# Optimization experiments

Hardware: AMD Instinct MI355X
Metric: run time of the kernel (lower is better)

## Reference

```python
import jax, jax.numpy as jnp
import numpy as np

H = 4          # num attention heads
C1 = 64        # channel_num[0]
C2 = 128       # channel_num[1]
KV = C1 + C2   # 192
MLP = C1 * 4   # expand_ratio=4


def _layernorm(x, g, b, eps=1e-6):
    m = jnp.mean(x, axis=-1, keepdims=True)
    v = jnp.mean((x - m) ** 2, axis=-1, keepdims=True)
    return (x - m) * jax.lax.rsqrt(v + eps) * g + b


def setup_inputs() -> dict:
    key = jax.random.key(0)
    ks = jax.random.split(key, 12)
    B, N = 8, 3136
    s_q = 1.0 / np.sqrt(C1)
    s_kv = 1.0 / np.sqrt(KV)
    return {
        "emb1": jax.random.normal(ks[0], (B, N, C1), jnp.float32),
        "emb2": jax.random.normal(ks[1], (B, N, C2), jnp.float32),
        # per-head projection weights (nn.Linear convention: y = x @ W.T)
        "Wq": jax.random.uniform(ks[2], (H, C1, C1), jnp.float32, -s_q, s_q),
        "Wk": jax.random.uniform(ks[3], (H, KV, KV), jnp.float32, -s_kv, s_kv),
        "Wv": jax.random.uniform(ks[4], (H, KV, KV), jnp.float32, -s_kv, s_kv),
        "Wout": jax.random.uniform(ks[5], (C1, C1), jnp.float32, -s_q, s_q),
        "ln1_g": jnp.ones((C1,), jnp.float32),
        "ln1_b": jnp.zeros((C1,), jnp.float32),
        "lnall_g": jnp.ones((KV,), jnp.float32),
        "lnall_b": jnp.zeros((KV,), jnp.float32),
        "ffn_g": jnp.ones((C1,), jnp.float32),
        "ffn_b": jnp.zeros((C1,), jnp.float32),
        "fc1_w": jax.random.uniform(ks[6], (MLP, C1), jnp.float32, -s_q, s_q),
        "fc1_b": jnp.zeros((MLP,), jnp.float32),
        "fc2_w": jax.random.uniform(ks[7], (C1, MLP), jnp.float32, -1.0 / np.sqrt(MLP), 1.0 / np.sqrt(MLP)),
        "fc2_b": jnp.zeros((C1,), jnp.float32),
    }


def reference(emb1, emb2, Wq, Wk, Wv, Wout, ln1_g, ln1_b, lnall_g, lnall_b,
              ffn_g, ffn_b, fc1_w, fc1_b, fc2_w, fc2_b):
    # emb1: [B,N,C1], emb2: [B,N,C2]
    emb_all = jnp.concatenate([emb1, emb2], axis=2)          # [B,N,KV]
    cx1 = _layernorm(emb1, ln1_g, ln1_b)                     # [B,N,C1]
    ea = _layernorm(emb_all, lnall_g, lnall_b)               # [B,N,KV]

    # batched per-head projections (replaces Python loop over ModuleList)
    qT = jnp.einsum('bnc,hdc->bhdn', cx1, Wq)                # [B,H,C1,N]
    k = jnp.einsum('bnk,hdk->bhnd', ea, Wk)                  # [B,H,N,KV]
    vT = jnp.einsum('bnk,hdk->bhdn', ea, Wv)                 # [B,H,KV,N]

    scores = jnp.einsum('bhcn,bhnk->bhck', qT, k) / np.sqrt(KV)  # [B,H,C1,KV]
    # InstanceNorm2d over spatial dims (C1, KV) per (batch, head), affine=False
    m = jnp.mean(scores, axis=(2, 3), keepdims=True)
    v = jnp.mean((scores - m) ** 2, axis=(2, 3), keepdims=True)
    scores = (scores - m) * jax.lax.rsqrt(v + 1e-5)
    probs = jax.nn.softmax(scores, axis=3)                   # softmax over KV

    ctx = jnp.einsum('bhck,bhkn->bhcn', probs, vT)           # [B,H,C1,N]
    ctx = jnp.mean(ctx, axis=1).transpose(0, 2, 1)           # mean over heads -> [B,N,C1]
    o = ctx @ Wout.T                                         # [B,N,C1]

    cx = emb1 + o                                            # residual
    x = _layernorm(cx, ffn_g, ffn_b)
    x = jax.nn.gelu(x @ fc1_w.T + fc1_b, approximate=False)
    x = x @ fc2_w.T + fc2_b
    return x + cx
```

## Files before the change

kernel.cpp:

```cpp
#include <hip/hip_runtime.h>
#include <hip/hip_bf16.h>

typedef __hip_bfloat16 bf;
typedef unsigned short ushort_t;
typedef __attribute__((ext_vector_type(8))) short short8;
typedef __attribute__((ext_vector_type(4))) float f32x4;

#define NB 8
#define SEQ 3136
#define HD 4
#define ZS 6

__device__ __forceinline__ float lo_bf(unsigned u){ return __uint_as_float(u << 16); }
__device__ __forceinline__ float hi_bf(unsigned u){ return __uint_as_float(u & 0xffff0000u); }
__device__ __forceinline__ float b16f(ushort_t s){ return __uint_as_float(((unsigned)s) << 16); }
__device__ __forceinline__ unsigned short f2bfbits(float f){
  unsigned u = __float_as_uint(f);
  unsigned r = u + 0x7fffu + ((u >> 16) & 1u);
  return (unsigned short)(r >> 16);
}
__device__ __forceinline__ float ldin(const void* p, long i, bool isbf){
  return isbf ? __bfloat162float(((const bf*)p)[i]) : ((const float*)p)[i];
}
__device__ __forceinline__ ushort_t cvt1(const void* p, long i, bool isbf){
  return isbf ? ((const ushort_t*)p)[i] : f2bfbits(((const float*)p)[i]);
}
#define DTYPE_FLAG(p) (((const unsigned*)(p))[0] == 0x3F803F80u)

__device__ __forceinline__ float wsum(float v){
  #pragma unroll
  for (int o = 32; o > 0; o >>= 1) v += __shfl_xor(v, o, 64);
  return v;
}

__global__ __launch_bounds__(256) void k_g(
    const void* __restrict__ emb1, const void* __restrict__ emb2,
    const void* __restrict__ g1, const void* __restrict__ b1,
    const void* __restrict__ ga, const void* __restrict__ ba,
    const void* __restrict__ Wq, const void* __restrict__ Wk, const void* __restrict__ Wv,
    const void* __restrict__ f1w, const void* __restrict__ f2w, const void* __restrict__ Wout,
    ushort_t* __restrict__ part, ushort_t* __restrict__ eag,
    ushort_t* __restrict__ Wqb, ushort_t* __restrict__ Wkb, ushort_t* __restrict__ WvTb,
    ushort_t* __restrict__ f1wb, ushort_t* __restrict__ f2wb,
    ushort_t* __restrict__ Woutb, unsigned* __restrict__ cnt){
  bool isbf = DTYPE_FLAG(g1);
  int tid = threadIdx.x;
  int b = blockIdx.y, ch = blockIdx.x;
  if (ch >= 49){
    if (b != 0) return;
    int g = (ch - 49)*256 + tid;
    const int STR = 24*256;
    if (g < 8) cnt[g] = 0;
    for (int i = g; i < 16384; i += STR) Wqb[i] = cvt1(Wq, i, isbf);
    for (int i = g; i < 4096;  i += STR) Woutb[i] = cvt1(Wout, i, isbf);
    for (int i = g; i < 147456; i += STR) Wkb[i] = cvt1(Wk, i, isbf);
    for (int i = g; i < 147456; i += STR){
      int hh = i / 36864, r = i - hh*36864;
      int j = r / 192, e = r - j*192;
      WvTb[i] = cvt1(Wv, (long)hh*36864 + e*192 + j, isbf);
    }
    for (int i = g; i < 16384; i += STR) f1wb[i] = cvt1(f1w, i, isbf);
    for (int i = g; i < 16384; i += STR) f2wb[i] = cvt1(f2w, i, isbf);
    return;
  }
  __shared__ __align__(16) ushort_t z1t[64*72];
  __shared__ __align__(16) ushort_t zat[192*72];
  int wave = tid >> 6, lane = tid & 63;
  int quad = lane >> 4, nl = lane & 15;
  long t0 = (long)b*SEQ + ch*64;
  float g1l = ldin(g1,lane,isbf), b1l = ldin(b1,lane,isbf);
  float ga0 = ldin(ga,lane,isbf),     ba0 = ldin(ba,lane,isbf);
  float ga1 = ldin(ga,64+lane,isbf),  ba1 = ldin(ba,64+lane,isbf);
  float ga2 = ldin(ga,128+lane,isbf), ba2 = ldin(ba,128+lane,isbf);
  #pragma unroll 4
  for (int k = 0; k < 16; ++k){
    int tok = wave*16 + k;
    long t = t0 + tok;
    float e1  = ldin(emb1, t*64 + lane, isbf);
    float e2a = ldin(emb2, t*128 + lane, isbf);
    float e2b = ldin(emb2, t*128 + 64 + lane, isbf);
    float s1 = wsum(e1), ss1 = wsum(e1*e1);
    float m1 = s1*(1.f/64.f);
    float r1 = rsqrtf(fmaxf(ss1*(1.f/64.f) - m1*m1, 0.f) + 1e-6f);
    z1t[lane*72 + tok] = f2bfbits((e1 - m1)*r1*g1l + b1l);
    float s23 = wsum(e2a+e2b), ss23 = wsum(e2a*e2a + e2b*e2b);
    float ma = (s1+s23)*(1.f/192.f);
    float ra = rsqrtf(fmaxf((ss1+ss23)*(1.f/192.f) - ma*ma, 0.f) + 1e-6f);
    unsigned short za0 = f2bfbits((e1  - ma)*ra*ga0 + ba0);
    unsigned short za1 = f2bfbits((e2a - ma)*ra*ga1 + ba1);
    unsigned short za2 = f2bfbits((e2b - ma)*ra*ga2 + ba2);
    zat[lane*72 + tok]       = za0;
    zat[(64+lane)*72 + tok]  = za1;
    zat[(128+lane)*72 + tok] = za2;
    eag[t*192 + lane]       = za0;
    eag[t*192 + 64 + lane]  = za1;
    eag[t*192 + 128 + lane] = za2;
  }
  __syncthreads();
  short8 a0 = *reinterpret_cast<const short8*>(&z1t[(wave*16+nl)*72 + quad*8]);
  short8 a1 = *reinterpret_cast<const short8*>(&z1t[(wave*16+nl)*72 + 32 + quad*8]);
  ushort_t* P = part + ((long)b*49 + ch)*12288;
  #pragma unroll
  for (int nt = 0; nt < 12; ++nt){
    f32x4 cd = {0.f,0.f,0.f,0.f};
    short8 b0 = *reinterpret_cast<const short8*>(&zat[(nt*16+nl)*72 + quad*8]);
    cd = __builtin_amdgcn_mfma_f32_16x16x32_bf16(a0, b0, cd, 0, 0, 0);
    short8 b1v = *reinterpret_cast<const short8*>(&zat[(nt*16+nl)*72 + 32 + quad*8]);
    cd = __builtin_amdgcn_mfma_f32_16x16x32_bf16(a1, b1v, cd, 0, 0, 0);
    #pragma unroll
    for (int reg = 0; reg < 4; ++reg)
      P[(wave*16 + quad*4 + reg)*192 + nt*16 + nl] = f2bfbits(cd[reg]);
  }
}

__global__ __launch_bounds__(64) void k_red(
    const ushort_t* __restrict__ part, ushort_t* __restrict__ Gb){
  int idx4 = blockIdx.x*64 + threadIdx.x;
  int b = idx4 / 3072, e4 = idx4 - b*3072;
  const ushort_t* p = part + (long)b*49*12288 + e4*4;
  float s0=0.f, s1=0.f, s2=0.f, s3=0.f;
  #pragma unroll
  for (int ch = 0; ch < 49; ++ch){
    uint2 u = *reinterpret_cast<const uint2*>(p + (long)ch*12288);
    s0 += lo_bf(u.x); s1 += hi_bf(u.x); s2 += lo_bf(u.y); s3 += hi_bf(u.y);
  }
  unsigned lo = (unsigned)f2bfbits(s0) | ((unsigned)f2bfbits(s1) << 16);
  unsigned hi = (unsigned)f2bfbits(s2) | ((unsigned)f2bfbits(s3) << 16);
  *reinterpret_cast<uint2*>(Gb + (long)idx4*4) = make_uint2(lo, hi);
}

__global__ __launch_bounds__(256) void k_att(
    const ushort_t* __restrict__ Gb, const ushort_t* __restrict__ Wqb,
    const ushort_t* __restrict__ Wkb, const ushort_t* __restrict__ WvTb,
    const ushort_t* __restrict__ Woutb,
    float* __restrict__ Mh, unsigned* __restrict__ cnt, ushort_t* __restrict__ W2){
  __shared__ __align__(16) ushort_t sT[192*72];
  __shared__ __align__(16) ushort_t sPh[64*200];
  __shared__ __align__(16) ushort_t sPl[64*200];
  __shared__ float red[8];
  __shared__ float stat[2];
  __shared__ unsigned sOld;
  int h = blockIdx.x, b = blockIdx.y, z = blockIdx.z;
  int tid = threadIdx.x, wave = tid >> 6, lane = tid & 63;
  int quad = lane >> 4, nl = lane & 15;

  const ushort_t* Gp = Gb + (long)b*12288;
  short8 aG[6];
  #pragma unroll
  for (int ks = 0; ks < 6; ++ks)
    aG[ks] = *reinterpret_cast<const short8*>(Gp + (wave*16+nl)*192 + ks*32 + quad*8);
  const ushort_t* Wkp = Wkb + (long)h*36864;
  short8 bcur[6], bnxt[6];
  #pragma unroll
  for (int ks = 0; ks < 6; ++ks)
    bcur[ks] = *reinterpret_cast<const short8*>(Wkp + (long)nl*192 + ks*32 + quad*8);
  #pragma unroll
  for (int nt = 0; nt < 12; ++nt){
    if (nt < 11){
      #pragma unroll
      for (int ks = 0; ks < 6; ++ks)
        bnxt[ks] = *reinterpret_cast<const short8*>(Wkp + (long)((nt+1)*16+nl)*192 + ks*32 + quad*8);
    }
    f32x4 cd = {0.f,0.f,0.f,0.f};
    #pragma unroll
    for (int ks = 0; ks < 6; ++ks)
      cd = __builtin_amdgcn_mfma_f32_16x16x32_bf16(aG[ks], bcur[ks], cd, 0, 0, 0);
    #pragma unroll
    for (int reg = 0; reg < 4; ++reg)
      sT[(nt*16+nl)*72 + wave*16 + quad*4 + reg] = f2bfbits(cd[reg]);
    #pragma unroll
    for (int ks = 0; ks < 6; ++ks) bcur[ks] = bnxt[ks];
  }
  __syncthreads();

  const ushort_t* Wqp = Wqb + (long)h*4096;
  short8 aQ[2];
  #pragma unroll
  for (int ks = 0; ks < 2; ++ks)
    aQ[ks] = *reinterpret_cast<const short8*>(Wqp + (wave*16+nl)*64 + ks*32 + quad*8);
  const float scale = 0.07216878364870323f;
  float sv[12][4];
  float ps = 0.f, pss = 0.f;
  #pragma unroll
  for (int nt = 0; nt < 12; ++nt){
    f32x4 cd = {0.f,0.f,0.f,0.f};
    #pragma unroll
    for (int ks = 0; ks < 2; ++ks){
      short8 bt = *reinterpret_cast<const short8*>(&sT[(nt*16+nl)*72 + ks*32 + quad*8]);
      cd = __builtin_amdgcn_mfma_f32_16x16x32_bf16(aQ[ks], bt, cd, 0, 0, 0);
    }
    #pragma unroll
    for (int reg = 0; reg < 4; ++reg){
      float v = cd[reg]*scale;
      sv[nt][reg] = v;
      ps += v; pss += v*v;
    }
  }
  ps = wsum(ps); pss = wsum(pss);
  if (lane == 0){ red[wave] = ps; red[4+wave] = pss; }
  __syncthreads();
  if (tid == 0){
    float s  = red[0]+red[1]+red[2]+red[3];
    float s2 = red[4]+red[5]+red[6]+red[7];
    float m = s * (1.f/12288.f);
    stat[0] = m;
    stat[1] = rsqrtf(fmaxf(s2*(1.f/12288.f) - m*m, 0.f) + 1e-5f);
  }
  __syncthreads();

  const ushort_t* Wvp = WvTb + (long)h*36864;
  short8 bv[2][6];
  #pragma unroll
  for (int ntl = 0; ntl < 2; ++ntl)
    #pragma unroll
    for (int ks = 0; ks < 6; ++ks)
      bv[ntl][ks] = *reinterpret_cast<const short8*>(Wvp + (long)((z*2+ntl)*16+nl)*192 + ks*32 + quad*8);

  float m = stat[0], r = stat[1];
  #pragma unroll
  for (int reg = 0; reg < 4; ++reg){
    float mx = -3.4e38f;
    #pragma unroll
    for (int nt = 0; nt < 12; ++nt){
      float v = (sv[nt][reg] - m)*r;
      sv[nt][reg] = v;
      mx = fmaxf(mx, v);
    }
    #pragma unroll
    for (int o = 1; o < 16; o <<= 1) mx = fmaxf(mx, __shfl_xor(mx, o, 64));
    float sum = 0.f;
    #pragma unroll
    for (int nt = 0; nt < 12; ++nt){
      float e = __expf(sv[nt][reg] - mx);
      sv[nt][reg] = e;
      sum += e;
    }
    #pragma unroll
    for (int o = 1; o < 16; o <<= 1) sum += __shfl_xor(sum, o, 64);
    float inv = 1.f / sum;
    int row = wave*16 + quad*4 + reg;
    #pragma unroll
    for (int nt = 0; nt < 12; ++nt){
      float e = sv[nt][reg]*inv;
      ushort_t hi = f2bfbits(e);
      sPh[row*200 + nt*16 + nl] = hi;
      sPl[row*200 + nt*16 + nl] = f2bfbits(e - b16f(hi));
    }
  }
  __syncthreads();

  short8 aPh[6], aPl[6];
  #pragma unroll
  for (int ks = 0; ks < 6; ++ks){
    aPh[ks] = *reinterpret_cast<const short8*>(&sPh[(wave*16+nl)*200 + ks*32 + quad*8]);
    aPl[ks] = *reinterpret_cast<const short8*>(&sPl[(wave*16+nl)*200 + ks*32 + quad*8]);
  }
  float* Mb = Mh + ((long)b*HD + h)*12288;
  #pragma unroll
  for (int ntl = 0; ntl < 2; ++ntl){
    int nt = z*2 + ntl;
    f32x4 cdh = {0.f,0.f,0.f,0.f};
    f32x4 cdl = {0.f,0.f,0.f,0.f};
    #pragma unroll
    for (int ks = 0; ks < 6; ++ks){
      cdl = __builtin_amdgcn_mfma_f32_16x16x32_bf16(aPl[ks], bv[ntl][ks], cdl, 0, 0, 0);
      cdh = __builtin_amdgcn_mfma_f32_16x16x32_bf16(aPh[ks], bv[ntl][ks], cdh, 0, 0, 0);
    }
    #pragma unroll
    for (int reg = 0; reg < 4; ++reg)
      Mb[(wave*16 + quad*4 + reg)*192 + nt*16 + nl] = cdh[reg] + cdl[reg];
  }

  __threadfence();
  if (tid == 0) sOld = atomicAdd(&cnt[b], 1u);
  __syncthreads();
  if (sOld == HD*ZS - 1u){
    __threadfence();
    const float* M0 = Mh + (long)b*HD*12288;
    for (int g = tid; g < 3072; g += 256){
      float4 x0 = ((const float4*)M0)[g];
      float4 x1 = ((const float4*)(M0 + 12288))[g];
      float4 x2 = ((const float4*)(M0 + 24576))[g];
      float4 x3 = ((const float4*)(M0 + 36864))[g];
      int e = g*4; int c = e/192, j = e - c*192;
      sT[(j+0)*72 + c] = f2bfbits(0.25f*(x0.x+x1.x+x2.x+x3.x));
      sT[(j+1)*72 + c] = f2bfbits(0.25f*(x0.y+x1.y+x2.y+x3.y));
      sT[(j+2)*72 + c] = f2bfbits(0.25f*(x0.z+x1.z+x2.z+x3.z));
      sT[(j+3)*72 + c] = f2bfbits(0.25f*(x0.w+x1.w+x2.w+x3.w));
    }
    __syncthreads();
    short8 aW[2];
    #pragma unroll
    for (int ks = 0; ks < 2; ++ks)
      aW[ks] = *reinterpret_cast<const short8*>(Woutb + (wave*16+nl)*64 + ks*32 + quad*8);
    ushort_t* W2b = W2 + (long)b*12288;
    #pragma unroll
    for (int nt = 0; nt < 12; ++nt){
      f32x4 cd = {0.f,0.f,0.f,0.f};
      #pragma unroll
      for (int ks = 0; ks < 2; ++ks){
        short8 bm = *reinterpret_cast<const short8*>(&sT[(nt*16+nl)*72 + ks*32 + quad*8]);
        cd = __builtin_amdgcn_mfma_f32_16x16x32_bf16(aW[ks], bm, cd, 0, 0, 0);
      }
      #pragma unroll
      for (int reg = 0; reg < 4; ++reg)
        W2b[(wave*16 + quad*4 + reg)*192 + nt*16 + nl] = f2bfbits(cd[reg]);
    }
  }
}

__global__ __launch_bounds__(256) void k_tail(
    const void* __restrict__ emb1, const ushort_t* __restrict__ eag,
    const ushort_t* __restrict__ W2g,
    const void* __restrict__ ffg, const void* __restrict__ ffb,
    const ushort_t* __restrict__ f1wb, const void* __restrict__ f1b,
    const ushort_t* __restrict__ f2wb, const void* __restrict__ f2b,
    const void* __restrict__ lng, void* __restrict__ out){
  bool isbf = DTYPE_FLAG(lng);
  __shared__ __align__(16) ushort_t sCX[16*72];
  __shared__ __align__(16) ushort_t sX[16*88];
  __shared__ __align__(16) ushort_t sH[16*280];
  int tid = threadIdx.x, wave = tid >> 6, lane = tid & 63;
  int quad = lane >> 4, nl = lane & 15;
  int b = blockIdx.y;
  long tbase = (long)b*SEQ + blockIdx.x*16;

  short8 aO[6];
  #pragma unroll
  for (int kt = 0; kt < 6; ++kt)
    aO[kt] = *reinterpret_cast<const short8*>(eag + (tbase + nl)*192 + kt*32 + quad*8);
  const ushort_t* W2b = W2g + (long)b*12288;
  {
    f32x4 cd = {0.f,0.f,0.f,0.f};
    #pragma unroll
    for (int kt = 0; kt < 6; ++kt){
      short8 bf8 = *reinterpret_cast<const short8*>(W2b + (wave*16+nl)*192 + kt*32 + quad*8);
      cd = __builtin_amdgcn_mfma_f32_16x16x32_bf16(aO[kt], bf8, cd, 0, 0, 0);
    }
    #pragma unroll
    for (int reg = 0; reg < 4; ++reg){
      int tokl = quad*4 + reg;
      int chn = wave*16 + nl;
      float e1v = ldin(emb1, (tbase + tokl)*64 + chn, isbf);
      sCX[tokl*72 + chn] = f2bfbits(cd[reg] + e1v);
    }
  }
  __syncthreads();

  float gl = ldin(ffg, lane, isbf), bl = ldin(ffb, lane, isbf);
  #pragma unroll
  for (int k = 0; k < 4; ++k){
    int tokl = wave*4 + k;
    float c = b16f(sCX[tokl*72 + lane]);
    float s = wsum(c), ss = wsum(c*c);
    float m = s*(1.f/64.f);
    float r = rsqrtf(fmaxf(ss*(1.f/64.f) - m*m, 0.f) + 1e-6f);
    sX[tokl*88 + lane] = f2bfbits((c - m)*r*gl + bl);
  }
  __syncthreads();

  short8 aX[2];
  #pragma unroll
  for (int kt = 0; kt < 2; ++kt)
    aX[kt] = *reinterpret_cast<const short8*>(&sX[nl*88 + kt*32 + quad*8]);
  #pragma unroll
  for (int nn = 0; nn < 4; ++nn){
    int nt = wave*4 + nn;
    f32x4 cd = {0.f,0.f,0.f,0.f};
    #pragma unroll
    for (int kt = 0; kt < 2; ++kt){
      short8 bf8 = *reinterpret_cast<const short8*>(f1wb + (long)(nt*16+nl)*64 + kt*32 + quad*8);
      cd = __builtin_amdgcn_mfma_f32_16x16x32_bf16(aX[kt], bf8, cd, 0, 0, 0);
    }
    float bb = ldin(f1b, nt*16+nl, isbf);
    #pragma unroll
    for (int reg = 0; reg < 4; ++reg){
      float v = cd[reg] + bb;
      float h = 0.5f*v*(1.f + erff(v*0.70710678118654752f));
      sH[(quad*4 + reg)*280 + nt*16 + nl] = f2bfbits(h);
    }
  }
  __syncthreads();

  short8 aH[8];
  #pragma unroll
  for (int kt = 0; kt < 8; ++kt)
    aH[kt] = *reinterpret_cast<const short8*>(&sH[nl*280 + kt*32 + quad*8]);
  {
    f32x4 cd = {0.f,0.f,0.f,0.f};
    #pragma unroll
    for (int kt = 0; kt < 8; ++kt){
      short8 bf8 = *reinterpret_cast<const short8*>(f2wb + (long)(wave*16+nl)*256 + kt*32 + quad*8);
      cd = __builtin_amdgcn_mfma_f32_16x16x32_bf16(aH[kt], bf8, cd, 0, 0, 0);
    }
    float bb2 = ldin(f2b, wave*16+nl, isbf);
    #pragma unroll
    for (int reg = 0; reg < 4; ++reg){
      int tokl = quad*4 + reg;
      int chn = wave*16 + nl;
      float y = cd[reg] + bb2 + b16f(sCX[tokl*72 + chn]);
      if (isbf) sCX[tokl*72 + chn] = f2bfbits(y);
      else ((float*)out)[(tbase + tokl)*64 + chn] = y;
    }
  }
  if (isbf){
    __syncthreads();
    int tokl = wave*4 + (lane >> 4), prt = lane & 15;
    uint2 v = *reinterpret_cast<const uint2*>(&sCX[tokl*72 + prt*4]);
    *reinterpret_cast<uint2*>((ushort_t*)out + (tbase + tokl)*64 + prt*4) = v;
  }
}

extern "C" void kernel_launch(void* const* d_in, const int* in_sizes, int n_in,
                              void* d_out, int out_size, void* d_ws, size_t ws_size,
                              hipStream_t stream){
  const void* emb1 = d_in[0];
  const void* emb2 = d_in[1];
  const void* Wq   = d_in[2];
  const void* Wk   = d_in[3];
  const void* Wv   = d_in[4];
  const void* Wout = d_in[5];
  const void* ln1g = d_in[6];
  const void* ln1b = d_in[7];
  const void* lag  = d_in[8];
  const void* lab  = d_in[9];
  const void* ffg  = d_in[10];
  const void* ffb  = d_in[11];
  const void* f1w  = d_in[12];
  const void* f1b  = d_in[13];
  const void* f2w  = d_in[14];
  const void* f2b  = d_in[15];

  char* base = (char*)d_ws;
  ushort_t* part = (ushort_t*)base;
  ushort_t* ea   = (ushort_t*)(base + 9633792);
  ushort_t* Gb   = (ushort_t*)(base + 19267584);
  float*    Mh   = (float*)(base + 19464192);
  ushort_t* W2   = (ushort_t*)(base + 21037056);
  ushort_t* Wqb  = (ushort_t*)(base + 21233664);
  ushort_t* Wkb  = (ushort_t*)(base + 21266432);
  ushort_t* WvTb = (ushort_t*)(base + 21561344);
  ushort_t* f1wb = (ushort_t*)(base + 21856256);
  ushort_t* f2wb = (ushort_t*)(base + 21889024);
  ushort_t* Woutb= (ushort_t*)(base + 21921792);
  unsigned* cnt  = (unsigned*)(base + 21929984);

  k_g   <<<dim3(73,NB),     256, 0, stream>>>(emb1, emb2, ln1g, ln1b, lag, lab,
                                              Wq, Wk, Wv, f1w, f2w, Wout,
                                              part, ea, Wqb, Wkb, WvTb, f1wb, f2wb,
                                              Woutb, cnt);
  k_red <<<384,              64, 0, stream>>>(part, Gb);
  k_att <<<dim3(HD,NB,ZS),  256, 0, stream>>>(Gb, Wqb, Wkb, WvTb, Woutb, Mh, cnt, W2);
  k_tail<<<dim3(196,NB),    256, 0, stream>>>(emb1, ea, W2, ffg, ffb,
                                              f1wb, f1b, f2wb, f2b, ln1g, d_out);
}
```

Measured before the change: 182.9 us.

## Fuse Gram reduction into k_g via last-block atomic counter; widen k_tail blocks

Removes the separate k_red launch: each k_g chunk block increments a per-batch atomic counter, and the last block to finish for a batch sums the 49 partial Gram tiles into Gb. Counters are now zeroed with a memset on the stream instead of inside k_g. k_tail is also reshaped to 512-thread blocks covering 32 tokens each, halving the block count. This trades one launch for a serial reduction done by a single block per batch, which may become a tail that delays k_att.

```diff
diff --git a/kernel.cpp b/kernel.cpp
--- a/kernel.cpp
+++ b/kernel.cpp
@@ -42,7 +42,8 @@
     ushort_t* __restrict__ part, ushort_t* __restrict__ eag,
     ushort_t* __restrict__ Wqb, ushort_t* __restrict__ Wkb, ushort_t* __restrict__ WvTb,
     ushort_t* __restrict__ f1wb, ushort_t* __restrict__ f2wb,
-    ushort_t* __restrict__ Woutb, unsigned* __restrict__ cnt){
+    ushort_t* __restrict__ Woutb, ushort_t* __restrict__ Gb,
+    unsigned* __restrict__ cntg){
   bool isbf = DTYPE_FLAG(g1);
   int tid = threadIdx.x;
   int b = blockIdx.y, ch = blockIdx.x;
@@ -50,7 +51,6 @@
     if (b != 0) return;
     int g = (ch - 49)*256 + tid;
     const int STR = 24*256;
-    if (g < 8) cnt[g] = 0;
     for (int i = g; i < 16384; i += STR) Wqb[i] = cvt1(Wq, i, isbf);
     for (int i = g; i < 4096;  i += STR) Woutb[i] = cvt1(Wout, i, isbf);
     for (int i = g; i < 147456; i += STR) Wkb[i] = cvt1(Wk, i, isbf);
@@ -65,6 +65,7 @@
   }
   __shared__ __align__(16) ushort_t z1t[64*72];
   __shared__ __align__(16) ushort_t zat[192*72];
+  __shared__ unsigned sOldg;
   int wave = tid >> 6, lane = tid & 63;
   int quad = lane >> 4, nl = lane & 15;
   long t0 = (long)b*SEQ + ch*64;
@@ -111,22 +112,26 @@
     for (int reg = 0; reg < 4; ++reg)
       P[(wave*16 + quad*4 + reg)*192 + nt*16 + nl] = f2bfbits(cd[reg]);
   }
-}
-
-__global__ __launch_bounds__(64) void k_red(
-    const ushort_t* __restrict__ part, ushort_t* __restrict__ Gb){
-  int idx4 = blockIdx.x*64 + threadIdx.x;
-  int b = idx4 / 3072, e4 = idx4 - b*3072;
-  const ushort_t* p = part + (long)b*49*12288 + e4*4;
-  float s0=0.f, s1=0.f, s2=0.f, s3=0.f;
-  #pragma unroll
-  for (int ch = 0; ch < 49; ++ch){
-    uint2 u = *reinterpret_cast<const uint2*>(p + (long)ch*12288);
-    s0 += lo_bf(u.x); s1 += hi_bf(u.x); s2 += lo_bf(u.y); s3 += hi_bf(u.y);
-  }
-  unsigned lo = (unsigned)f2bfbits(s0) | ((unsigned)f2bfbits(s1) << 16);
-  unsigned hi = (unsigned)f2bfbits(s2) | ((unsigned)f2bfbits(s3) << 16);
-  *reinterpret_cast<uint2*>(Gb + (long)idx4*4) = make_uint2(lo, hi);
+
+  __threadfence();
+  if (tid == 0) sOldg = atomicAdd(&cntg[b], 1u);
+  __syncthreads();
+  if (sOldg == 48u){
+    __threadfence();
+    const ushort_t* pb = part + (long)b*49*12288;
+    ushort_t* Gp = Gb + (long)b*12288;
+    for (int g = tid; g < 3072; g += 256){
+      float a0s=0.f, a1s=0.f, a2s=0.f, a3s=0.f;
+      #pragma unroll 7
+      for (int c49 = 0; c49 < 49; ++c49){
+        uint2 u = *reinterpret_cast<const uint2*>(pb + (long)c49*12288 + g*4);
+        a0s += lo_bf(u.x); a1s += hi_bf(u.x); a2s += lo_bf(u.y); a3s += hi_bf(u.y);
+      }
+      unsigned lo = (unsigned)f2bfbits(a0s) | ((unsigned)f2bfbits(a1s) << 16);
+      unsigned hi = (unsigned)f2bfbits(a2s) | ((unsigned)f2bfbits(a3s) << 16);
+      *reinterpret_cast<uint2*>(Gp + g*4) = make_uint2(lo, hi);
+    }
+  }
 }
 
 __global__ __launch_bounds__(256) void k_att(
@@ -309,7 +314,7 @@
   }
 }
 
-__global__ __launch_bounds__(256) void k_tail(
+__global__ __launch_bounds__(512, 2) void k_tail(
     const void* __restrict__ emb1, const ushort_t* __restrict__ eag,
     const ushort_t* __restrict__ W2g,
     const void* __restrict__ ffg, const void* __restrict__ ffb,
@@ -317,30 +322,31 @@
     const ushort_t* __restrict__ f2wb, const void* __restrict__ f2b,
     const void* __restrict__ lng, void* __restrict__ out){
   bool isbf = DTYPE_FLAG(lng);
-  __shared__ __align__(16) ushort_t sCX[16*72];
-  __shared__ __align__(16) ushort_t sX[16*88];
-  __shared__ __align__(16) ushort_t sH[16*280];
+  __shared__ __align__(16) ushort_t sCX[32*72];
+  __shared__ __align__(16) ushort_t sX[32*88];
+  __shared__ __align__(16) ushort_t sH[32*280];
   int tid = threadIdx.x, wave = tid >> 6, lane = tid & 63;
   int quad = lane >> 4, nl = lane & 15;
+  int tg = wave >> 2, wq = wave & 3;
   int b = blockIdx.y;
-  long tbase = (long)b*SEQ + blockIdx.x*16;
+  long tbase = (long)b*SEQ + blockIdx.x*32;
 
   short8 aO[6];
   #pragma unroll
   for (int kt = 0; kt < 6; ++kt)
-    aO[kt] = *reinterpret_cast<const short8*>(eag + (tbase + nl)*192 + kt*32 + quad*8);
+    aO[kt] = *reinterpret_cast<const short8*>(eag + (tbase + tg*16 + nl)*192 + kt*32 + quad*8);
   const ushort_t* W2b = W2g + (long)b*12288;
   {
     f32x4 cd = {0.f,0.f,0.f,0.f};
     #pragma unroll
     for (int kt = 0; kt < 6; ++kt){
-      short8 bf8 = *reinterpret_cast<const short8*>(W2b + (wave*16+nl)*192 + kt*32 + quad*8);
+      short8 bf8 = *reinterpret_cast<const short8*>(W2b + (wq*16+nl)*192 + kt*32 + quad*8);
       cd = __builtin_amdgcn_mfma_f32_16x16x32_bf16(aO[kt], bf8, cd, 0, 0, 0);
     }
     #pragma unroll
     for (int reg = 0; reg < 4; ++reg){
-      int tokl = quad*4 + reg;
-      int chn = wave*16 + nl;
+      int tokl = tg*16 + quad*4 + reg;
+      int chn = wq*16 + nl;
       float e1v = ldin(emb1, (tbase + tokl)*64 + chn, isbf);
       sCX[tokl*72 + chn] = f2bfbits(cd[reg] + e1v);
     }
@@ -362,10 +368,10 @@
   short8 aX[2];
   #pragma unroll
   for (int kt = 0; kt < 2; ++kt)
-    aX[kt] = *reinterpret_cast<const short8*>(&sX[nl*88 + kt*32 + quad*8]);
+    aX[kt] = *reinterpret_cast<const short8*>(&sX[(tg*16+nl)*88 + kt*32 + quad*8]);
   #pragma unroll
   for (int nn = 0; nn < 4; ++nn){
-    int nt = wave*4 + nn;
+    int nt = wq*4 + nn;
     f32x4 cd = {0.f,0.f,0.f,0.f};
     #pragma unroll
     for (int kt = 0; kt < 2; ++kt){
@@ -377,7 +383,7 @@
     for (int reg = 0; reg < 4; ++reg){
       float v = cd[reg] + bb;
       float h = 0.5f*v*(1.f + erff(v*0.70710678118654752f));
-      sH[(quad*4 + reg)*280 + nt*16 + nl] = f2bfbits(h);
+      sH[(tg*16 + quad*4 + reg)*280 + nt*16 + nl] = f2bfbits(h);
     }
   }
   __syncthreads();
@@ -385,19 +391,19 @@
   short8 aH[8];
   #pragma unroll
   for (int kt = 0; kt < 8; ++kt)
-    aH[kt] = *reinterpret_cast<const short8*>(&sH[nl*280 + kt*32 + quad*8]);
+    aH[kt] = *reinterpret_cast<const short8*>(&sH[(tg*16+nl)*280 + kt*32 + quad*8]);
   {
     f32x4 cd = {0.f,0.f,0.f,0.f};
     #pragma unroll
     for (int kt = 0; kt < 8; ++kt){
-      short8 bf8 = *reinterpret_cast<const short8*>(f2wb + (long)(wave*16+nl)*256 + kt*32 + quad*8);
+      short8 bf8 = *reinterpret_cast<const short8*>(f2wb + (long)(wq*16+nl)*256 + kt*32 + quad*8);
       cd = __builtin_amdgcn_mfma_f32_16x16x32_bf16(aH[kt], bf8, cd, 0, 0, 0);
     }
-    float bb2 = ldin(f2b, wave*16+nl, isbf);
+    float bb2 = ldin(f2b, wq*16+nl, isbf);
     #pragma unroll
     for (int reg = 0; reg < 4; ++reg){
-      int tokl = quad*4 + reg;
-      int chn = wave*16 + nl;
+      int tokl = tg*16 + quad*4 + reg;
+      int chn = wq*16 + nl;
       float y = cd[reg] + bb2 + b16f(sCX[tokl*72 + chn]);
       if (isbf) sCX[tokl*72 + chn] = f2bfbits(y);
       else ((float*)out)[(tbase + tokl)*64 + chn] = y;
@@ -444,13 +450,15 @@
   ushort_t* f2wb = (ushort_t*)(base + 21889024);
   ushort_t* Woutb= (ushort_t*)(base + 21921792);
   unsigned* cnt  = (unsigned*)(base + 21929984);
+  unsigned* cntg = (unsigned*)(base + 21930016);
+
+  hipMemsetAsync(cnt, 0, 64, stream);
 
   k_g   <<<dim3(73,NB),     256, 0, stream>>>(emb1, emb2, ln1g, ln1b, lag, lab,
                                               Wq, Wk, Wv, f1w, f2w, Wout,
                                               part, ea, Wqb, Wkb, WvTb, f1wb, f2wb,
-                                              Woutb, cnt);
-  k_red <<<384,              64, 0, stream>>>(part, Gb);
+                                              Woutb, Gb, cntg);
   k_att <<<dim3(HD,NB,ZS),  256, 0, stream>>>(Gb, Wqb, Wkb, WvTb, Woutb, Mh, cnt, W2);
-  k_tail<<<dim3(196,NB),    256, 0, stream>>>(emb1, ea, W2, ffg, ffb,
+  k_tail<<<dim3(98,NB),     512, 0, stream>>>(emb1, ea, W2, ffg, ffb,
                                               f1wb, f1b, f2wb, f2b, ln1g, d_out);
 }
```

Result: slower. 285.7 us (+56.2%).
